# Kernel tuning notes

Measured on AMD Instinct MI355X. Metric: run time of the kernel, lower is better.

Reference implementation:

```python
import jax, jax.numpy as jnp
import numpy as np

N_NODES = 100000
N_EDGES = 1600000
IN_H = 18        # n_rw + 2
NHID_STR = 256
OUT_H = 11       # max(1, int(18/64*40))
NCLASS = 40


def gcn_conv(x, edge_index, W, b, num_nodes):
    """PyG GCNConv: add self-loops, symmetric norm, gather-matmul-scatter."""
    x = x @ W  # [N, out]
    loops = jnp.arange(num_nodes, dtype=edge_index.dtype)
    src = jnp.concatenate([edge_index[0], loops])
    dst = jnp.concatenate([edge_index[1], loops])
    deg = jax.ops.segment_sum(jnp.ones_like(dst, dtype=x.dtype), dst,
                              num_segments=num_nodes)
    dinv = jnp.where(deg > 0, jax.lax.rsqrt(deg), 0.0)
    norm = dinv[src] * dinv[dst]  # [E+N]
    msgs = x[src] * norm[:, None]  # gather + scale
    out = jax.ops.segment_sum(msgs, dst, num_segments=num_nodes)
    return out + b


def setup_inputs() -> dict:
    key = jax.random.key(0)
    ks = jax.random.split(key, 10)
    stc_enc = jax.random.normal(ks[0], (N_NODES, IN_H), dtype=jnp.float32)
    edge_index = jax.random.randint(ks[1], (2, N_EDGES), 0, N_NODES, dtype=jnp.int64)
    emb_a = jax.random.normal(ks[2], (N_NODES, NCLASS), dtype=jnp.float32)
    # Glorot-ish params
    W1 = jax.random.normal(ks[3], (IN_H, NHID_STR), dtype=jnp.float32) / np.sqrt(IN_H)
    b1 = jnp.zeros((NHID_STR,), dtype=jnp.float32)
    W2 = jax.random.normal(ks[4], (NHID_STR, OUT_H), dtype=jnp.float32) / np.sqrt(NHID_STR)
    b2 = jnp.zeros((OUT_H,), dtype=jnp.float32)
    Wc = jax.random.normal(ks[5], (NCLASS + OUT_H, NCLASS), dtype=jnp.float32) / np.sqrt(NCLASS + OUT_H)
    bc = jnp.zeros((NCLASS,), dtype=jnp.float32)
    return {"stc_enc": stc_enc, "edge_index": edge_index, "emb_a": emb_a,
            "W1": W1, "b1": b1, "W2": W2, "b2": b2, "Wc": Wc, "bc": bc}


def reference(stc_enc, edge_index, emb_a, W1, b1, W2, b2, Wc, bc):
    # eval mode: F.dropout(training=False) is identity
    h = gcn_conv(stc_enc, edge_index, W1, b1, N_NODES)
    h = gcn_conv(h, edge_index, W2, b2, N_NODES)
    emb_b = jax.nn.relu(h)
    emb = jnp.concatenate([emb_a, emb_b], axis=-1)  # [N, nclass+out_h]
    return emb @ Wc + bc
```

## Files before the change

kernel.cpp:

```cpp
#include <hip/hip_runtime.h>

#define N_NODES 100000
#define N_EDGES 1600000
#define IN_H 18
#define OUT_H 11
#define NCLASS 40
#define NHID 256

#define BBITS 9
#define BINS 512
#define NB 196
#define NBLK 800
#define CHUNK 2000
#define SRC_MASK 0x1FFFF

__device__ __forceinline__ float bflo(unsigned u) { return __uint_as_float(u << 16); }
__device__ __forceinline__ float bfhi(unsigned u) { return __uint_as_float(u & 0xFFFF0000u); }
__device__ __forceinline__ unsigned bfr(float x) {
    unsigned u = __float_as_uint(x);
    return (u + 0x7FFFu + ((u >> 16) & 1u)) >> 16;
}
__device__ __forceinline__ unsigned bfpack(float a, float b) { return bfr(a) | (bfr(b) << 16); }
__device__ __forceinline__ float4 bfunpack4(uint2 w) {
    return make_float4(bflo(w.x), bfhi(w.x), bflo(w.y), bfhi(w.y));
}

__global__ void k_hist(const int* __restrict__ dst, int* __restrict__ bh, int E) {
    __shared__ int h[NB];
    int t = threadIdx.x;
    if (t < NB) h[t] = 0;
    __syncthreads();
    const int4* d4 = (const int4*)(dst + blockIdx.x * CHUNK);
    for (int i = t; i < CHUNK / 4; i += blockDim.x) {
        int4 w = d4[i];
        atomicAdd(&h[w.x >> BBITS], 1);
        atomicAdd(&h[w.y >> BBITS], 1);
        atomicAdd(&h[w.z >> BBITS], 1);
        atomicAdd(&h[w.w >> BBITS], 1);
    }
    __syncthreads();
    if (t < NB) bh[t * NBLK + blockIdx.x] = h[t];
}

__global__ void k_btot(const int* __restrict__ bh, int* __restrict__ btot) {
    __shared__ int s[256];
    int b = blockIdx.x, t = threadIdx.x;
    int sum = 0;
    for (int k = t; k < NBLK; k += 256) sum += bh[b * NBLK + k];
    s[t] = sum;
    __syncthreads();
    for (int off = 128; off > 0; off >>= 1) {
        if (t < off) s[t] += s[t + off];
        __syncthreads();
    }
    if (t == 0) btot[b] = s[0];
}

__global__ __launch_bounds__(1024) void k_boff(int* __restrict__ bh,
                                               const int* __restrict__ btot,
                                               int* __restrict__ bstart) {
    __shared__ int s0[1024], s1[1024];
    __shared__ int bt0[256], bt1[256];
    int b = blockIdx.x, t = threadIdx.x;
    if (t < 256) bt0[t] = (t < NB) ? btot[t] : 0;
    __syncthreads();
    int* c0 = bt0; int* c1 = bt1;
    for (int off = 1; off < 256; off <<= 1) {
        if (t < 256) c1[t] = c0[t] + ((t >= off) ? c0[t - off] : 0);
        __syncthreads();
        int* tmp = c0; c0 = c1; c1 = tmp;
    }
    int base = c0[b] - btot[b];
    if (t == 0) {
        bstart[b] = base;
        if (b == 0) bstart[NB] = N_EDGES;
    }
    int v = (t < NBLK) ? bh[b * NBLK + t] : 0;
    s0[t] = v;
    __syncthreads();
    int* c = s0; int* n = s1;
    for (int off = 1; off < 1024; off <<= 1) {
        n[t] = c[t] + ((t >= off) ? c[t - off] : 0);
        __syncthreads();
        int* tmp = c; c = n; n = tmp;
    }
    if (t < NBLK) bh[b * NBLK + t] = c[t] - v + base;
}

__global__ void k_bucket(const int* __restrict__ ei, const int* __restrict__ bh,
                         unsigned int* __restrict__ packed, int E) {
    __shared__ int cur[NB];
    int t = threadIdx.x;
    if (t < NB) cur[t] = bh[t * NBLK + blockIdx.x];
    __syncthreads();
    int base = blockIdx.x * CHUNK;
    const int4* s4 = (const int4*)(ei + base);
    const int4* d4 = (const int4*)(ei + E + base);
    for (int i = t; i < CHUNK / 4; i += blockDim.x) {
        int4 s = s4[i];
        int4 d = d4[i];
        int sl;
        sl = atomicAdd(&cur[d.x >> BBITS], 1);
        packed[sl] = ((unsigned)(d.x & (BINS - 1)) << 17) | (unsigned)s.x;
        sl = atomicAdd(&cur[d.y >> BBITS], 1);
        packed[sl] = ((unsigned)(d.y & (BINS - 1)) << 17) | (unsigned)s.y;
        sl = atomicAdd(&cur[d.z >> BBITS], 1);
        packed[sl] = ((unsigned)(d.z & (BINS - 1)) << 17) | (unsigned)s.z;
        sl = atomicAdd(&cur[d.w >> BBITS], 1);
        packed[sl] = ((unsigned)(d.w & (BINS - 1)) << 17) | (unsigned)s.w;
    }
}

__global__ void k_w12(const float* __restrict__ W1, const float* __restrict__ b1,
                      const float* __restrict__ W2,
                      float* __restrict__ W12, float* __restrict__ bb) {
    int t = threadIdx.x;
    if (t < IN_H * OUT_H) {
        int i = t / OUT_H, j = t % OUT_H;
        float s = 0.f;
        for (int k = 0; k < NHID; ++k) s += W1[i * NHID + k] * W2[k * OUT_H + j];
        W12[t] = s;
    } else if (t < IN_H * OUT_H + OUT_H) {
        int j = t - IN_H * OUT_H;
        float s = 0.f;
        for (int k = 0; k < NHID; ++k) s += b1[k] * W2[k * OUT_H + j];
        bb[j] = s;
    }
}

__global__ __launch_bounds__(1024)
void k_sort(const unsigned int* __restrict__ packed, const int* __restrict__ bstart,
            const float* __restrict__ X, const float* __restrict__ W12g,
            int* __restrict__ col, int* __restrict__ rowptr,
            float* __restrict__ dinv, unsigned int* __restrict__ Pp) {
    __shared__ int hist[BINS];
    __shared__ int s0[BINS], s1[BINS];
    __shared__ int cur[BINS];
    __shared__ float sW[IN_H * OUT_H];
    int b = blockIdx.x, t = threadIdx.x;
    int beg = bstart[b], end = bstart[b + 1];
    if (t < BINS) hist[t] = 0;
    if (t >= BINS && t < BINS + IN_H * OUT_H) sW[t - BINS] = W12g[t - BINS];
    __syncthreads();
    for (int i = beg + t; i < end; i += blockDim.x)
        atomicAdd(&hist[packed[i] >> 17], 1);
    __syncthreads();
    if (t < BINS) s0[t] = hist[t];
    __syncthreads();
    int* c = s0; int* n = s1;
    for (int off = 1; off < BINS; off <<= 1) {
        if (t < BINS) n[t] = c[t] + ((t >= off) ? c[t - off] : 0);
        __syncthreads();
        int* tmp = c; c = n; n = tmp;
    }
    if (t < BINS) {
        int excl = c[t] - hist[t];
        int gbase = beg + excl;
        cur[t] = gbase;
        int node = (b << BBITS) + t;
        if (node <= N_NODES) rowptr[node] = gbase;
        if (node < N_NODES)  dinv[node] = rsqrtf((float)(hist[t] + 1));
    }
    __syncthreads();
    for (int i = beg + t; i < end; i += blockDim.x) {
        unsigned p = packed[i];
        int slot = atomicAdd(&cur[p >> 17], 1);
        col[slot] = (int)(p & SRC_MASK);
    }
    int node = (b << BBITS) + t;
    if (t < BINS && node < N_NODES) {
        float dv = rsqrtf((float)(hist[t] + 1));
        float x[IN_H];
        const float2* xr = (const float2*)(X + (size_t)node * IN_H);
        #pragma unroll
        for (int k = 0; k < IN_H / 2; ++k) {
            float2 cc = xr[k];
            x[2 * k] = cc.x; x[2 * k + 1] = cc.y;
        }
        float pf[12];
        #pragma unroll
        for (int j = 0; j < OUT_H; ++j) {
            float s = 0.f;
            #pragma unroll
            for (int k = 0; k < IN_H; ++k) s += x[k] * sW[k * OUT_H + j];
            pf[j] = dv * s;
        }
        pf[11] = dv;
        uint4* pw = (uint4*)(Pp + (size_t)node * 8);
        pw[0] = make_uint4(bfpack(pf[0], pf[1]), bfpack(pf[2], pf[3]),
                           bfpack(pf[4], pf[5]), bfpack(pf[6], pf[7]));
        pw[1] = make_uint4(bfpack(pf[8], pf[9]), bfpack(pf[10], pf[11]), 0u, 0u);
    }
}

__global__ void k_gather1(const int* __restrict__ rowptr, const int* __restrict__ col,
                          const float* __restrict__ dinv, const unsigned int* __restrict__ Pp,
                          unsigned int* __restrict__ Z1p, float* __restrict__ r, int n) {
    int g = blockIdx.x * blockDim.x + threadIdx.x;
    int v = g >> 2;
    int lane = g & 3;
    if (v >= n) return;
    int beg = rowptr[v], end = rowptr[v + 1];
    float4 acc = make_float4(0.f, 0.f, 0.f, 0.f);
    const uint2* P2 = (const uint2*)Pp;
    int e = beg;
    for (; e + 3 < end; e += 4) {
        int i0 = col[e], i1 = col[e + 1], i2 = col[e + 2], i3 = col[e + 3];
        uint2 w0 = P2[(size_t)i0 * 4 + lane];
        uint2 w1 = P2[(size_t)i1 * 4 + lane];
        uint2 w2 = P2[(size_t)i2 * 4 + lane];
        uint2 w3 = P2[(size_t)i3 * 4 + lane];
        float4 a0 = bfunpack4(w0), a1 = bfunpack4(w1), a2 = bfunpack4(w2), a3 = bfunpack4(w3);
        acc.x += a0.x + a1.x + a2.x + a3.x;
        acc.y += a0.y + a1.y + a2.y + a3.y;
        acc.z += a0.z + a1.z + a2.z + a3.z;
        acc.w += a0.w + a1.w + a2.w + a3.w;
    }
    for (; e < end; ++e) {
        float4 a = bfunpack4(P2[(size_t)col[e] * 4 + lane]);
        acc.x += a.x; acc.y += a.y; acc.z += a.z; acc.w += a.w;
    }
    {
        float4 a = bfunpack4(P2[(size_t)v * 4 + lane]);
        acc.x += a.x; acc.y += a.y; acc.z += a.z; acc.w += a.w;
    }
    float dd = dinv[v];
    float s2 = dd * dd;
    ((uint2*)Z1p)[(size_t)v * 4 + lane] =
        make_uint2(bfpack(s2 * acc.x, s2 * acc.y), bfpack(s2 * acc.z, s2 * acc.w));
    if (lane == 2) r[v] = dd * acc.w;
}

__global__ void k_g2d(const int* __restrict__ rowptr, const int* __restrict__ col,
                      const float* __restrict__ dinv, const unsigned int* __restrict__ Z1p,
                      const float* __restrict__ r, const float* __restrict__ bbg,
                      const float* __restrict__ b2g, const float* __restrict__ emb_a,
                      const float* __restrict__ Wc, const float* __restrict__ bc,
                      float* __restrict__ out, int n) {
    __shared__ float sWc[(NCLASS + OUT_H) * NCLASS];
    __shared__ float sbc[NCLASS];
    __shared__ float sbb[16];
    __shared__ float sb2[16];
    for (int t = threadIdx.x; t < (NCLASS + OUT_H) * NCLASS; t += blockDim.x) sWc[t] = Wc[t];
    if (threadIdx.x < NCLASS) sbc[threadIdx.x] = bc[threadIdx.x];
    if (threadIdx.x < 16) {
        sbb[threadIdx.x] = (threadIdx.x < OUT_H) ? bbg[threadIdx.x] : 0.f;
        sb2[threadIdx.x] = (threadIdx.x < OUT_H) ? b2g[threadIdx.x] : 0.f;
    }
    __syncthreads();
    int g = blockIdx.x * blockDim.x + threadIdx.x;
    int v = g >> 2;
    int lane = g & 3;
    if (v >= n) return;
    int beg = rowptr[v], end = rowptr[v + 1];
    float4 acc = make_float4(0.f, 0.f, 0.f, 0.f);
    const uint2* Z2 = (const uint2*)Z1p;
    int e = beg;
    for (; e + 3 < end; e += 4) {
        int i0 = col[e], i1 = col[e + 1], i2 = col[e + 2], i3 = col[e + 3];
        uint2 w0 = Z2[(size_t)i0 * 4 + lane];
        uint2 w1 = Z2[(size_t)i1 * 4 + lane];
        uint2 w2 = Z2[(size_t)i2 * 4 + lane];
        uint2 w3 = Z2[(size_t)i3 * 4 + lane];
        float4 a0 = bfunpack4(w0), a1 = bfunpack4(w1), a2 = bfunpack4(w2), a3 = bfunpack4(w3);
        acc.x += a0.x + a1.x + a2.x + a3.x;
        acc.y += a0.y + a1.y + a2.y + a3.y;
        acc.z += a0.z + a1.z + a2.z + a3.z;
        acc.w += a0.w + a1.w + a2.w + a3.w;
    }
    for (; e < end; ++e) {
        float4 a = bfunpack4(Z2[(size_t)col[e] * 4 + lane]);
        acc.x += a.x; acc.y += a.y; acc.z += a.z; acc.w += a.w;
    }
    {
        float4 a = bfunpack4(Z2[(size_t)v * 4 + lane]);
        acc.x += a.x; acc.y += a.y; acc.z += a.z; acc.w += a.w;
    }
    float dd = dinv[v];
    float rv = r[v];
    float af[4] = {acc.x, acc.y, acc.z, acc.w};
    float hloc[4];
    #pragma unroll
    for (int c = 0; c < 4; ++c) {
        int f = 4 * lane + c;
        float tv = dd * af[c] + rv * sbb[f] + sb2[f];
        hloc[c] = tv > 0.f ? tv : 0.f;
    }
    float hall[OUT_H];
    #pragma unroll
    for (int f = 0; f < OUT_H; ++f)
        hall[f] = __shfl(hloc[f & 3], f >> 2, 4);
    const int jb = 10 * lane;
    float o[10];
    #pragma unroll
    for (int j = 0; j < 10; ++j) o[j] = sbc[jb + j];
    const float4* ea4 = (const float4*)(emb_a + (size_t)v * NCLASS);
    #pragma unroll
    for (int k4 = 0; k4 < NCLASS / 4; ++k4) {
        float4 a = ea4[k4];
        const float* w0 = &sWc[(4 * k4 + 0) * NCLASS + jb];
        const float* w1 = &sWc[(4 * k4 + 1) * NCLASS + jb];
        const float* w2 = &sWc[(4 * k4 + 2) * NCLASS + jb];
        const float* w3 = &sWc[(4 * k4 + 3) * NCLASS + jb];
        #pragma unroll
        for (int j = 0; j < 10; ++j)
            o[j] += a.x * w0[j] + a.y * w1[j] + a.z * w2[j] + a.w * w3[j];
    }
    #pragma unroll
    for (int f = 0; f < OUT_H; ++f) {
        const float* w = &sWc[(NCLASS + f) * NCLASS + jb];
        float hv = hall[f];
        #pragma unroll
        for (int j = 0; j < 10; ++j) o[j] += hv * w[j];
    }
    float* orow = out + (size_t)v * NCLASS + jb;
    #pragma unroll
    for (int j2 = 0; j2 < 5; ++j2)
        *(float2*)(orow + 2 * j2) = make_float2(o[2 * j2], o[2 * j2 + 1]);
}

extern "C" void kernel_launch(void* const* d_in, const int* in_sizes, int n_in,
                              void* d_out, int out_size, void* d_ws, size_t ws_size,
                              hipStream_t stream) {
    const float* X     = (const float*)d_in[0];
    const int*   ei    = (const int*)d_in[1];
    const float* emb_a = (const float*)d_in[2];
    const float* W1    = (const float*)d_in[3];
    const float* b1    = (const float*)d_in[4];
    const float* W2    = (const float*)d_in[5];
    const float* b2    = (const float*)d_in[6];
    const float* Wc    = (const float*)d_in[7];
    const float* bc    = (const float*)d_in[8];
    float* out = (float*)d_out;

    char* ws = (char*)d_ws;
    size_t off = 0;
    auto alloc = [&](size_t nbytes) {
        void* p = (void*)(ws + off);
        off += ((nbytes + 255) / 256) * 256;
        return p;
    };
    char* bh_base = (char*)alloc((size_t)NB * NBLK * sizeof(int));
    int*   bh     = (int*)bh_base;
    float* rvec   = (float*)bh_base;
    int*   btot   = (int*)  alloc(NB * sizeof(int));
    int*   bstart = (int*)  alloc((NB + 1) * sizeof(int));
    unsigned int* packed = (unsigned int*)alloc((size_t)N_EDGES * sizeof(unsigned int));
    int*   col    = (int*)  alloc((size_t)N_EDGES * sizeof(int));
    int*   rowptr = (int*)  alloc((N_NODES + 1) * sizeof(int));
    float* dinv   = (float*)alloc(N_NODES * sizeof(float));
    float* W12    = (float*)alloc(IN_H * OUT_H * sizeof(float));
    float* bb     = (float*)alloc(OUT_H * sizeof(float));
    unsigned int* Pp  = (unsigned int*)alloc((size_t)N_NODES * 32);
    unsigned int* Z1p = (unsigned int*)alloc((size_t)N_NODES * 32);

    const int B = 256;
    int gN4 = (N_NODES * 4 + B - 1) / B;

    k_w12    <<<1, B, 0, stream>>>(W1, b1, W2, W12, bb);
    k_hist   <<<NBLK, B, 0, stream>>>(ei + N_EDGES, bh, N_EDGES);
    k_btot   <<<NB, 256, 0, stream>>>(bh, btot);
    k_boff   <<<NB, 1024, 0, stream>>>(bh, btot, bstart);
    k_bucket <<<NBLK, B, 0, stream>>>(ei, bh, packed, N_EDGES);
    k_sort   <<<NB, 1024, 0, stream>>>(packed, bstart, X, W12, col, rowptr, dinv, Pp);
    k_gather1<<<gN4, B, 0, stream>>>(rowptr, col, dinv, Pp, Z1p, rvec, N_NODES);
    k_g2d    <<<gN4, B, 0, stream>>>(rowptr, col, dinv, Z1p, rvec, bb, b2, emb_a,
                                     Wc, bc, out, N_NODES);
}
```

Before: 112.6 us.

## Replace CSR sort and per-node gathers with bucketed LDS-atomic propagation

The per-bucket counting sort that built col/rowptr is removed. Both GCN propagation passes now stream the bucketed packed edge list directly and accumulate the 12 bf16-decoded features per destination node with shared-memory float atomics. The bucket width drops from 512 to 128 nodes, so there are 782 buckets and the accumulator fits in LDS; histogram and offset kernels are adapted with strided loops and a larger scan. This saves the second sort pass and the col/rowptr traffic. In exchange it adds many LDS atomics and makes float summation order nondeterministic.

```diff
diff --git a/kernel.cpp b/kernel.cpp
--- a/kernel.cpp
+++ b/kernel.cpp
@@ -7,12 +7,13 @@
 #define NCLASS 40
 #define NHID 256
 
-#define BBITS 9
-#define BINS 512
-#define NB 196
+#define BBITS 7
+#define BINS 128
+#define NB 782
 #define NBLK 800
 #define CHUNK 2000
 #define SRC_MASK 0x1FFFF
+#define DMASK (BINS - 1)
 
 __device__ __forceinline__ float bflo(unsigned u) { return __uint_as_float(u << 16); }
 __device__ __forceinline__ float bfhi(unsigned u) { return __uint_as_float(u & 0xFFFF0000u); }
@@ -21,17 +22,23 @@
     return (u + 0x7FFFu + ((u >> 16) & 1u)) >> 16;
 }
 __device__ __forceinline__ unsigned bfpack(float a, float b) { return bfr(a) | (bfr(b) << 16); }
-__device__ __forceinline__ float4 bfunpack4(uint2 w) {
-    return make_float4(bflo(w.x), bfhi(w.x), bflo(w.y), bfhi(w.y));
+
+__device__ __forceinline__ void lds_acc12(float* a, uint4 w0, uint2 w1) {
+    atomicAdd(a + 0,  bflo(w0.x)); atomicAdd(a + 1,  bfhi(w0.x));
+    atomicAdd(a + 2,  bflo(w0.y)); atomicAdd(a + 3,  bfhi(w0.y));
+    atomicAdd(a + 4,  bflo(w0.z)); atomicAdd(a + 5,  bfhi(w0.z));
+    atomicAdd(a + 6,  bflo(w0.w)); atomicAdd(a + 7,  bfhi(w0.w));
+    atomicAdd(a + 8,  bflo(w1.x)); atomicAdd(a + 9,  bfhi(w1.x));
+    atomicAdd(a + 10, bflo(w1.y)); atomicAdd(a + 11, bfhi(w1.y));
 }
 
 __global__ void k_hist(const int* __restrict__ dst, int* __restrict__ bh, int E) {
     __shared__ int h[NB];
     int t = threadIdx.x;
-    if (t < NB) h[t] = 0;
+    for (int i = t; i < NB; i += 256) h[i] = 0;
     __syncthreads();
     const int4* d4 = (const int4*)(dst + blockIdx.x * CHUNK);
-    for (int i = t; i < CHUNK / 4; i += blockDim.x) {
+    for (int i = t; i < CHUNK / 4; i += 256) {
         int4 w = d4[i];
         atomicAdd(&h[w.x >> BBITS], 1);
         atomicAdd(&h[w.y >> BBITS], 1);
@@ -39,7 +46,7 @@
         atomicAdd(&h[w.w >> BBITS], 1);
     }
     __syncthreads();
-    if (t < NB) bh[t * NBLK + blockIdx.x] = h[t];
+    for (int i = t; i < NB; i += 256) bh[i * NBLK + blockIdx.x] = h[i];
 }
 
 __global__ void k_btot(const int* __restrict__ bh, int* __restrict__ btot) {
@@ -60,13 +67,13 @@
                                                const int* __restrict__ btot,
                                                int* __restrict__ bstart) {
     __shared__ int s0[1024], s1[1024];
-    __shared__ int bt0[256], bt1[256];
-    int b = blockIdx.x, t = threadIdx.x;
-    if (t < 256) bt0[t] = (t < NB) ? btot[t] : 0;
-    __syncthreads();
-    int* c0 = bt0; int* c1 = bt1;
-    for (int off = 1; off < 256; off <<= 1) {
-        if (t < 256) c1[t] = c0[t] + ((t >= off) ? c0[t - off] : 0);
+    __shared__ int bt0[1024], bt1[1024];
+    int b = blockIdx.x, t = threadIdx.x;
+    bt0[t] = (t < NB) ? btot[t] : 0;
+    __syncthreads();
+    int *c0 = bt0, *c1 = bt1;
+    for (int off = 1; off < 1024; off <<= 1) {
+        c1[t] = c0[t] + ((t >= off) ? c0[t - off] : 0);
         __syncthreads();
         int* tmp = c0; c0 = c1; c1 = tmp;
     }
@@ -78,7 +85,7 @@
     int v = (t < NBLK) ? bh[b * NBLK + t] : 0;
     s0[t] = v;
     __syncthreads();
-    int* c = s0; int* n = s1;
+    int *c = s0, *n = s1;
     for (int off = 1; off < 1024; off <<= 1) {
         n[t] = c[t] + ((t >= off) ? c[t - off] : 0);
         __syncthreads();
@@ -91,23 +98,23 @@
                          unsigned int* __restrict__ packed, int E) {
     __shared__ int cur[NB];
     int t = threadIdx.x;
-    if (t < NB) cur[t] = bh[t * NBLK + blockIdx.x];
+    for (int i = t; i < NB; i += 256) cur[i] = bh[i * NBLK + blockIdx.x];
     __syncthreads();
     int base = blockIdx.x * CHUNK;
     const int4* s4 = (const int4*)(ei + base);
     const int4* d4 = (const int4*)(ei + E + base);
-    for (int i = t; i < CHUNK / 4; i += blockDim.x) {
+    for (int i = t; i < CHUNK / 4; i += 256) {
         int4 s = s4[i];
         int4 d = d4[i];
         int sl;
         sl = atomicAdd(&cur[d.x >> BBITS], 1);
-        packed[sl] = ((unsigned)(d.x & (BINS - 1)) << 17) | (unsigned)s.x;
+        packed[sl] = ((unsigned)(d.x & DMASK) << 17) | (unsigned)s.x;
         sl = atomicAdd(&cur[d.y >> BBITS], 1);
-        packed[sl] = ((unsigned)(d.y & (BINS - 1)) << 17) | (unsigned)s.y;
+        packed[sl] = ((unsigned)(d.y & DMASK) << 17) | (unsigned)s.y;
         sl = atomicAdd(&cur[d.z >> BBITS], 1);
-        packed[sl] = ((unsigned)(d.z & (BINS - 1)) << 17) | (unsigned)s.z;
+        packed[sl] = ((unsigned)(d.z & DMASK) << 17) | (unsigned)s.z;
         sl = atomicAdd(&cur[d.w >> BBITS], 1);
-        packed[sl] = ((unsigned)(d.w & (BINS - 1)) << 17) | (unsigned)s.w;
+        packed[sl] = ((unsigned)(d.w & DMASK) << 17) | (unsigned)s.w;
     }
 }
 
@@ -128,195 +135,175 @@
     }
 }
 
-__global__ __launch_bounds__(1024)
-void k_sort(const unsigned int* __restrict__ packed, const int* __restrict__ bstart,
+__global__ __launch_bounds__(512)
+void k_prep(const unsigned int* __restrict__ packed, const int* __restrict__ bstart,
             const float* __restrict__ X, const float* __restrict__ W12g,
-            int* __restrict__ col, int* __restrict__ rowptr,
             float* __restrict__ dinv, unsigned int* __restrict__ Pp) {
     __shared__ int hist[BINS];
-    __shared__ int s0[BINS], s1[BINS];
-    __shared__ int cur[BINS];
     __shared__ float sW[IN_H * OUT_H];
     int b = blockIdx.x, t = threadIdx.x;
-    int beg = bstart[b], end = bstart[b + 1];
     if (t < BINS) hist[t] = 0;
     if (t >= BINS && t < BINS + IN_H * OUT_H) sW[t - BINS] = W12g[t - BINS];
     __syncthreads();
-    for (int i = beg + t; i < end; i += blockDim.x)
-        atomicAdd(&hist[packed[i] >> 17], 1);
-    __syncthreads();
-    if (t < BINS) s0[t] = hist[t];
-    __syncthreads();
-    int* c = s0; int* n = s1;
-    for (int off = 1; off < BINS; off <<= 1) {
-        if (t < BINS) n[t] = c[t] + ((t >= off) ? c[t - off] : 0);
-        __syncthreads();
-        int* tmp = c; c = n; n = tmp;
-    }
+    int beg = bstart[b], end = bstart[b + 1];
+    for (int i = beg + t; i < end; i += 512)
+        atomicAdd(&hist[(packed[i] >> 17) & DMASK], 1);
+    __syncthreads();
     if (t < BINS) {
-        int excl = c[t] - hist[t];
-        int gbase = beg + excl;
-        cur[t] = gbase;
         int node = (b << BBITS) + t;
-        if (node <= N_NODES) rowptr[node] = gbase;
-        if (node < N_NODES)  dinv[node] = rsqrtf((float)(hist[t] + 1));
-    }
-    __syncthreads();
-    for (int i = beg + t; i < end; i += blockDim.x) {
-        unsigned p = packed[i];
-        int slot = atomicAdd(&cur[p >> 17], 1);
-        col[slot] = (int)(p & SRC_MASK);
-    }
-    int node = (b << BBITS) + t;
-    if (t < BINS && node < N_NODES) {
-        float dv = rsqrtf((float)(hist[t] + 1));
-        float x[IN_H];
-        const float2* xr = (const float2*)(X + (size_t)node * IN_H);
-        #pragma unroll
-        for (int k = 0; k < IN_H / 2; ++k) {
-            float2 cc = xr[k];
-            x[2 * k] = cc.x; x[2 * k + 1] = cc.y;
-        }
-        float pf[12];
-        #pragma unroll
-        for (int j = 0; j < OUT_H; ++j) {
-            float s = 0.f;
-            #pragma unroll
-            for (int k = 0; k < IN_H; ++k) s += x[k] * sW[k * OUT_H + j];
-            pf[j] = dv * s;
-        }
-        pf[11] = dv;
-        uint4* pw = (uint4*)(Pp + (size_t)node * 8);
-        pw[0] = make_uint4(bfpack(pf[0], pf[1]), bfpack(pf[2], pf[3]),
-                           bfpack(pf[4], pf[5]), bfpack(pf[6], pf[7]));
-        pw[1] = make_uint4(bfpack(pf[8], pf[9]), bfpack(pf[10], pf[11]), 0u, 0u);
-    }
-}
-
-__global__ void k_gather1(const int* __restrict__ rowptr, const int* __restrict__ col,
-                          const float* __restrict__ dinv, const unsigned int* __restrict__ Pp,
-                          unsigned int* __restrict__ Z1p, float* __restrict__ r, int n) {
-    int g = blockIdx.x * blockDim.x + threadIdx.x;
-    int v = g >> 2;
-    int lane = g & 3;
-    if (v >= n) return;
-    int beg = rowptr[v], end = rowptr[v + 1];
-    float4 acc = make_float4(0.f, 0.f, 0.f, 0.f);
-    const uint2* P2 = (const uint2*)Pp;
-    int e = beg;
-    for (; e + 3 < end; e += 4) {
-        int i0 = col[e], i1 = col[e + 1], i2 = col[e + 2], i3 = col[e + 3];
-        uint2 w0 = P2[(size_t)i0 * 4 + lane];
-        uint2 w1 = P2[(size_t)i1 * 4 + lane];
-        uint2 w2 = P2[(size_t)i2 * 4 + lane];
-        uint2 w3 = P2[(size_t)i3 * 4 + lane];
-        float4 a0 = bfunpack4(w0), a1 = bfunpack4(w1), a2 = bfunpack4(w2), a3 = bfunpack4(w3);
-        acc.x += a0.x + a1.x + a2.x + a3.x;
-        acc.y += a0.y + a1.y + a2.y + a3.y;
-        acc.z += a0.z + a1.z + a2.z + a3.z;
-        acc.w += a0.w + a1.w + a2.w + a3.w;
-    }
-    for (; e < end; ++e) {
-        float4 a = bfunpack4(P2[(size_t)col[e] * 4 + lane]);
-        acc.x += a.x; acc.y += a.y; acc.z += a.z; acc.w += a.w;
-    }
-    {
-        float4 a = bfunpack4(P2[(size_t)v * 4 + lane]);
-        acc.x += a.x; acc.y += a.y; acc.z += a.z; acc.w += a.w;
-    }
-    float dd = dinv[v];
-    float s2 = dd * dd;
-    ((uint2*)Z1p)[(size_t)v * 4 + lane] =
-        make_uint2(bfpack(s2 * acc.x, s2 * acc.y), bfpack(s2 * acc.z, s2 * acc.w));
-    if (lane == 2) r[v] = dd * acc.w;
-}
-
-__global__ void k_g2d(const int* __restrict__ rowptr, const int* __restrict__ col,
-                      const float* __restrict__ dinv, const unsigned int* __restrict__ Z1p,
-                      const float* __restrict__ r, const float* __restrict__ bbg,
-                      const float* __restrict__ b2g, const float* __restrict__ emb_a,
-                      const float* __restrict__ Wc, const float* __restrict__ bc,
-                      float* __restrict__ out, int n) {
+        if (node < N_NODES) {
+            float dv = rsqrtf((float)(hist[t] + 1));
+            dinv[node] = dv;
+            float x[IN_H];
+            const float2* xr = (const float2*)(X + (size_t)node * IN_H);
+            #pragma unroll
+            for (int k = 0; k < IN_H / 2; ++k) {
+                float2 cc = xr[k];
+                x[2 * k] = cc.x; x[2 * k + 1] = cc.y;
+            }
+            float pf[OUT_H];
+            #pragma unroll
+            for (int j = 0; j < OUT_H; ++j) {
+                float s = 0.f;
+                #pragma unroll
+                for (int k = 0; k < IN_H; ++k) s += x[k] * sW[k * OUT_H + j];
+                pf[j] = dv * s;
+            }
+            unsigned* pr = Pp + (size_t)node * 8;
+            ((uint4*)pr)[0] = make_uint4(bfpack(pf[0], pf[1]), bfpack(pf[2], pf[3]),
+                                         bfpack(pf[4], pf[5]), bfpack(pf[6], pf[7]));
+            ((uint4*)pr)[1] = make_uint4(bfpack(pf[8], pf[9]), bfpack(pf[10], dv), 0u, 0u);
+        }
+    }
+}
+
+__global__ __launch_bounds__(512)
+void k_prop1(const unsigned int* __restrict__ packed, const int* __restrict__ bstart,
+             const float* __restrict__ dinv, const unsigned int* __restrict__ Pp,
+             unsigned int* __restrict__ Z1p, float* __restrict__ rvec) {
+    __shared__ float acc[BINS * 12];
+    int b = blockIdx.x, t = threadIdx.x;
+    for (int i = t; i < BINS * 12; i += 512) acc[i] = 0.f;
+    __syncthreads();
+    int beg = bstart[b], end = bstart[b + 1];
+    int e = beg + t;
+    for (; e + 512 < end; e += 1024) {
+        unsigned p0 = packed[e], p1 = packed[e + 512];
+        const unsigned* r0 = Pp + (size_t)(p0 & SRC_MASK) * 8;
+        const unsigned* r1 = Pp + (size_t)(p1 & SRC_MASK) * 8;
+        uint4 w00 = ((const uint4*)r0)[0]; uint2 w01 = *(const uint2*)(r0 + 4);
+        uint4 w10 = ((const uint4*)r1)[0]; uint2 w11 = *(const uint2*)(r1 + 4);
+        lds_acc12(&acc[((p0 >> 17) & DMASK) * 12], w00, w01);
+        lds_acc12(&acc[((p1 >> 17) & DMASK) * 12], w10, w11);
+    }
+    if (e < end) {
+        unsigned p = packed[e];
+        const unsigned* r = Pp + (size_t)(p & SRC_MASK) * 8;
+        uint4 w0 = ((const uint4*)r)[0]; uint2 w1 = *(const uint2*)(r + 4);
+        lds_acc12(&acc[((p >> 17) & DMASK) * 12], w0, w1);
+    }
+    __syncthreads();
+    if (t < BINS) {
+        int node = (b << BBITS) + t;
+        if (node < N_NODES) {
+            float dd = dinv[node];
+            const unsigned* pr = Pp + (size_t)node * 8;
+            uint4 w0 = ((const uint4*)pr)[0]; uint2 w1 = *(const uint2*)(pr + 4);
+            float sf[12] = {bflo(w0.x), bfhi(w0.x), bflo(w0.y), bfhi(w0.y),
+                            bflo(w0.z), bfhi(w0.z), bflo(w0.w), bfhi(w0.w),
+                            bflo(w1.x), bfhi(w1.x), bflo(w1.y), bfhi(w1.y)};
+            float z[12];
+            #pragma unroll
+            for (int j = 0; j < 12; ++j) z[j] = acc[t * 12 + j] + sf[j];
+            float s2 = dd * dd;
+            rvec[node] = dd * z[11];
+            unsigned* zr = Z1p + (size_t)node * 8;
+            ((uint4*)zr)[0] = make_uint4(bfpack(s2 * z[0], s2 * z[1]), bfpack(s2 * z[2], s2 * z[3]),
+                                         bfpack(s2 * z[4], s2 * z[5]), bfpack(s2 * z[6], s2 * z[7]));
+            ((uint4*)zr)[1] = make_uint4(bfpack(s2 * z[8], s2 * z[9]), bfpack(s2 * z[10], 0.f), 0u, 0u);
+        }
+    }
+}
+
+__global__ __launch_bounds__(512)
+void k_prop2(const unsigned int* __restrict__ packed, const int* __restrict__ bstart,
+             const float* __restrict__ dinv, const unsigned int* __restrict__ Z1p,
+             const float* __restrict__ rvec, const float* __restrict__ bbg,
+             const float* __restrict__ b2g, const float* __restrict__ emb_a,
+             const float* __restrict__ Wc, const float* __restrict__ bc,
+             float* __restrict__ out) {
+    __shared__ float acc[BINS * 12];
     __shared__ float sWc[(NCLASS + OUT_H) * NCLASS];
     __shared__ float sbc[NCLASS];
-    __shared__ float sbb[16];
-    __shared__ float sb2[16];
-    for (int t = threadIdx.x; t < (NCLASS + OUT_H) * NCLASS; t += blockDim.x) sWc[t] = Wc[t];
-    if (threadIdx.x < NCLASS) sbc[threadIdx.x] = bc[threadIdx.x];
-    if (threadIdx.x < 16) {
-        sbb[threadIdx.x] = (threadIdx.x < OUT_H) ? bbg[threadIdx.x] : 0.f;
-        sb2[threadIdx.x] = (threadIdx.x < OUT_H) ? b2g[threadIdx.x] : 0.f;
-    }
-    __syncthreads();
-    int g = blockIdx.x * blockDim.x + threadIdx.x;
-    int v = g >> 2;
-    int lane = g & 3;
-    if (v >= n) return;
-    int beg = rowptr[v], end = rowptr[v + 1];
-    float4 acc = make_float4(0.f, 0.f, 0.f, 0.f);
-    const uint2* Z2 = (const uint2*)Z1p;
-    int e = beg;
-    for (; e + 3 < end; e += 4) {
-        int i0 = col[e], i1 = col[e + 1], i2 = col[e + 2], i3 = col[e + 3];
-        uint2 w0 = Z2[(size_t)i0 * 4 + lane];
-        uint2 w1 = Z2[(size_t)i1 * 4 + lane];
-        uint2 w2 = Z2[(size_t)i2 * 4 + lane];
-        uint2 w3 = Z2[(size_t)i3 * 4 + lane];
-        float4 a0 = bfunpack4(w0), a1 = bfunpack4(w1), a2 = bfunpack4(w2), a3 = bfunpack4(w3);
-        acc.x += a0.x + a1.x + a2.x + a3.x;
-        acc.y += a0.y + a1.y + a2.y + a3.y;
-        acc.z += a0.z + a1.z + a2.z + a3.z;
-        acc.w += a0.w + a1.w + a2.w + a3.w;
-    }
-    for (; e < end; ++e) {
-        float4 a = bfunpack4(Z2[(size_t)col[e] * 4 + lane]);
-        acc.x += a.x; acc.y += a.y; acc.z += a.z; acc.w += a.w;
-    }
-    {
-        float4 a = bfunpack4(Z2[(size_t)v * 4 + lane]);
-        acc.x += a.x; acc.y += a.y; acc.z += a.z; acc.w += a.w;
-    }
-    float dd = dinv[v];
-    float rv = r[v];
-    float af[4] = {acc.x, acc.y, acc.z, acc.w};
-    float hloc[4];
-    #pragma unroll
-    for (int c = 0; c < 4; ++c) {
-        int f = 4 * lane + c;
-        float tv = dd * af[c] + rv * sbb[f] + sb2[f];
-        hloc[c] = tv > 0.f ? tv : 0.f;
-    }
-    float hall[OUT_H];
-    #pragma unroll
-    for (int f = 0; f < OUT_H; ++f)
-        hall[f] = __shfl(hloc[f & 3], f >> 2, 4);
-    const int jb = 10 * lane;
-    float o[10];
-    #pragma unroll
-    for (int j = 0; j < 10; ++j) o[j] = sbc[jb + j];
-    const float4* ea4 = (const float4*)(emb_a + (size_t)v * NCLASS);
-    #pragma unroll
-    for (int k4 = 0; k4 < NCLASS / 4; ++k4) {
-        float4 a = ea4[k4];
-        const float* w0 = &sWc[(4 * k4 + 0) * NCLASS + jb];
-        const float* w1 = &sWc[(4 * k4 + 1) * NCLASS + jb];
-        const float* w2 = &sWc[(4 * k4 + 2) * NCLASS + jb];
-        const float* w3 = &sWc[(4 * k4 + 3) * NCLASS + jb];
-        #pragma unroll
-        for (int j = 0; j < 10; ++j)
-            o[j] += a.x * w0[j] + a.y * w1[j] + a.z * w2[j] + a.w * w3[j];
-    }
-    #pragma unroll
-    for (int f = 0; f < OUT_H; ++f) {
-        const float* w = &sWc[(NCLASS + f) * NCLASS + jb];
-        float hv = hall[f];
-        #pragma unroll
-        for (int j = 0; j < 10; ++j) o[j] += hv * w[j];
-    }
-    float* orow = out + (size_t)v * NCLASS + jb;
-    #pragma unroll
-    for (int j2 = 0; j2 < 5; ++j2)
-        *(float2*)(orow + 2 * j2) = make_float2(o[2 * j2], o[2 * j2 + 1]);
+    __shared__ float sbb[OUT_H];
+    __shared__ float sb2[OUT_H];
+    int b = blockIdx.x, t = threadIdx.x;
+    for (int i = t; i < BINS * 12; i += 512) acc[i] = 0.f;
+    for (int i = t; i < (NCLASS + OUT_H) * NCLASS; i += 512) sWc[i] = Wc[i];
+    if (t < NCLASS) sbc[t] = bc[t];
+    if (t < OUT_H) { sbb[t] = bbg[t]; sb2[t] = b2g[t]; }
+    __syncthreads();
+    int beg = bstart[b], end = bstart[b + 1];
+    int e = beg + t;
+    for (; e + 512 < end; e += 1024) {
+        unsigned p0 = packed[e], p1 = packed[e + 512];
+        const unsigned* r0 = Z1p + (size_t)(p0 & SRC_MASK) * 8;
+        const unsigned* r1 = Z1p + (size_t)(p1 & SRC_MASK) * 8;
+        uint4 w00 = ((const uint4*)r0)[0]; uint2 w01 = *(const uint2*)(r0 + 4);
+        uint4 w10 = ((const uint4*)r1)[0]; uint2 w11 = *(const uint2*)(r1 + 4);
+        lds_acc12(&acc[((p0 >> 17) & DMASK) * 12], w00, w01);
+        lds_acc12(&acc[((p1 >> 17) & DMASK) * 12], w10, w11);
+    }
+    if (e < end) {
+        unsigned p = packed[e];
+        const unsigned* r = Z1p + (size_t)(p & SRC_MASK) * 8;
+        uint4 w0 = ((const uint4*)r)[0]; uint2 w1 = *(const uint2*)(r + 4);
+        lds_acc12(&acc[((p >> 17) & DMASK) * 12], w0, w1);
+    }
+    __syncthreads();
+    int tn = t >> 2, jh = (t & 3) * 10;
+    int node = (b << BBITS) + tn;
+    if (node < N_NODES) {
+        float dd = dinv[node], rv = rvec[node];
+        const unsigned* zr = Z1p + (size_t)node * 8;
+        uint4 w0 = ((const uint4*)zr)[0]; uint2 w1 = *(const uint2*)(zr + 4);
+        float zf[11] = {bflo(w0.x), bfhi(w0.x), bflo(w0.y), bfhi(w0.y),
+                        bflo(w0.z), bfhi(w0.z), bflo(w0.w), bfhi(w0.w),
+                        bflo(w1.x), bfhi(w1.x), bflo(w1.y)};
+        const float* ap = &acc[tn * 12];
+        float h[OUT_H];
+        #pragma unroll
+        for (int f = 0; f < OUT_H; ++f) {
+            float tv = dd * (ap[f] + zf[f]) + rv * sbb[f] + sb2[f];
+            h[f] = tv > 0.f ? tv : 0.f;
+        }
+        float o[10];
+        #pragma unroll
+        for (int j = 0; j < 10; ++j) o[j] = sbc[jh + j];
+        const float4* ea4 = (const float4*)(emb_a + (size_t)node * NCLASS);
+        #pragma unroll
+        for (int k4 = 0; k4 < NCLASS / 4; ++k4) {
+            float4 a = ea4[k4];
+            const float* q0 = &sWc[(4 * k4 + 0) * NCLASS + jh];
+            const float* q1 = &sWc[(4 * k4 + 1) * NCLASS + jh];
+            const float* q2 = &sWc[(4 * k4 + 2) * NCLASS + jh];
+            const float* q3 = &sWc[(4 * k4 + 3) * NCLASS + jh];
+            #pragma unroll
+            for (int j = 0; j < 10; ++j)
+                o[j] += a.x * q0[j] + a.y * q1[j] + a.z * q2[j] + a.w * q3[j];
+        }
+        #pragma unroll
+        for (int f = 0; f < OUT_H; ++f) {
+            const float* q = &sWc[(NCLASS + f) * NCLASS + jh];
+            float hv = h[f];
+            #pragma unroll
+            for (int j = 0; j < 10; ++j) o[j] += hv * q[j];
+        }
+        float* orow = out + (size_t)node * NCLASS + jh;
+        #pragma unroll
+        for (int j2 = 0; j2 < 5; ++j2)
+            *(float2*)(orow + 2 * j2) = make_float2(o[2 * j2], o[2 * j2 + 1]);
+    }
 }
 
 extern "C" void kernel_launch(void* const* d_in, const int* in_sizes, int n_in,
@@ -346,24 +333,19 @@
     int*   btot   = (int*)  alloc(NB * sizeof(int));
     int*   bstart = (int*)  alloc((NB + 1) * sizeof(int));
     unsigned int* packed = (unsigned int*)alloc((size_t)N_EDGES * sizeof(unsigned int));
-    int*   col    = (int*)  alloc((size_t)N_EDGES * sizeof(int));
-    int*   rowptr = (int*)  alloc((N_NODES + 1) * sizeof(int));
     float* dinv   = (float*)alloc(N_NODES * sizeof(float));
     float* W12    = (float*)alloc(IN_H * OUT_H * sizeof(float));
     float* bb     = (float*)alloc(OUT_H * sizeof(float));
     unsigned int* Pp  = (unsigned int*)alloc((size_t)N_NODES * 32);
     unsigned int* Z1p = (unsigned int*)alloc((size_t)N_NODES * 32);
 
-    const int B = 256;
-    int gN4 = (N_NODES * 4 + B - 1) / B;
-
-    k_w12    <<<1, B, 0, stream>>>(W1, b1, W2, W12, bb);
-    k_hist   <<<NBLK, B, 0, stream>>>(ei + N_EDGES, bh, N_EDGES);
-    k_btot   <<<NB, 256, 0, stream>>>(bh, btot);
-    k_boff   <<<NB, 1024, 0, stream>>>(bh, btot, bstart);
-    k_bucket <<<NBLK, B, 0, stream>>>(ei, bh, packed, N_EDGES);
-    k_sort   <<<NB, 1024, 0, stream>>>(packed, bstart, X, W12, col, rowptr, dinv, Pp);
-    k_gather1<<<gN4, B, 0, stream>>>(rowptr, col, dinv, Pp, Z1p, rvec, N_NODES);
-    k_g2d    <<<gN4, B, 0, stream>>>(rowptr, col, dinv, Z1p, rvec, bb, b2, emb_a,
-                                     Wc, bc, out, N_NODES);
-}
+    k_w12   <<<1, 256, 0, stream>>>(W1, b1, W2, W12, bb);
+    k_hist  <<<NBLK, 256, 0, stream>>>(ei + N_EDGES, bh, N_EDGES);
+    k_btot  <<<NB, 256, 0, stream>>>(bh, btot);
+    k_boff  <<<NB, 1024, 0, stream>>>(bh, btot, bstart);
+    k_bucket<<<NBLK, 256, 0, stream>>>(ei, bh, packed, N_EDGES);
+    k_prep  <<<NB, 512, 0, stream>>>(packed, bstart, X, W12, dinv, Pp);
+    k_prop1 <<<NB, 512, 0, stream>>>(packed, bstart, dinv, Pp, Z1p, rvec);
+    k_prop2 <<<NB, 512, 0, stream>>>(packed, bstart, dinv, Z1p, rvec, bb, b2, emb_a,
+                                     Wc, bc, out);
+}
```

Result: slower. 345.6 us (+207.0%).
